# Kernel tuning notes

Hardware: AMD Instinct MI355X
Metric: run time of the kernel (lower is better)

Reference implementation:

```python
import jax, jax.numpy as jnp
import numpy as np

B, S, D, H = 2, 2048, 1024, 16
HD = D // H  # 64
SOFT_CAP = 50.0
MAX_WAVELENGTH = 10000.0


def apply_rope(x, positions, head_dim):
    # x: [B,S,H,hd], positions: [B,S]
    fraction = 2.0 * jnp.arange(head_dim // 2, dtype=jnp.float32) / head_dim
    timescale = MAX_WAVELENGTH ** fraction                      # [hd/2]
    sinusoid = positions.astype(jnp.float32)[..., None] / timescale  # [B,S,hd/2]
    sin = jnp.sin(sinusoid)[..., None, :]                       # [B,S,1,hd/2]
    cos = jnp.cos(sinusoid)[..., None, :]
    first, second = jnp.split(x, 2, axis=-1)
    out = jnp.concatenate(
        [first * cos - second * sin, second * cos + first * sin], axis=-1)
    return out.astype(x.dtype)


def setup_inputs() -> dict:
    key = jax.random.key(0)
    k1, k2, k3 = jax.random.split(key, 3)
    inputs = jax.random.normal(k1, (B, S, D), jnp.float32)
    segment_positions = jnp.tile(jnp.arange(S, dtype=jnp.int32), (B, 1))
    mask = jnp.tril(jnp.ones((S, S), dtype=bool))[None, None]   # causal [1,1,S,S]
    w_in = jax.random.normal(k2, (D, H, 3 * HD), jnp.float32) * 0.02
    w_out = jax.random.normal(k3, (H, HD, D), jnp.float32) * 0.02
    return {"inputs": inputs, "segment_positions": segment_positions,
            "mask": mask, "w_in": w_in, "w_out": w_out}


def reference(inputs, segment_positions, mask, w_in, w_out):
    # fused QKV projection: [B,S,H,3*hd]
    proj = jnp.einsum('bsd,dhe->bshe', inputs, w_in)
    q, k, v = jnp.split(proj, 3, axis=-1)
    q = apply_rope(q, segment_positions, HD)
    k = apply_rope(k, segment_positions, HD)
    q = q / jnp.sqrt(jnp.float32(HD))
    attn = jnp.einsum('bqhd,bkhd->bhqk', q, k)                  # [B,H,S,S]
    big_neg = jnp.finfo(jnp.float32).min
    attn = jnp.where(mask, attn, big_neg)
    attn = jnp.tanh(attn / SOFT_CAP) * SOFT_CAP                 # soft-cap AFTER mask
    attn = jax.nn.softmax(attn, axis=-1)
    x = jnp.einsum('bhqk,bkhd->bqhd', attn, v)
    return jnp.einsum('bqhd,hdo->bqo', x, w_out)
```

## Files before the change

kernel.cpp:

```cpp
#include <hip/hip_runtime.h>
#include <math.h>

#define BB 2
#define SS 2048
#define DD 1024
#define HH 16
#define HDIM 64
#define BS (BB*SS)
#define NQKV (HH*3*HDIM)
#define PERHEAD ((size_t)SS*HDIM)

typedef __attribute__((ext_vector_type(8))) short bf16x8;
typedef __attribute__((ext_vector_type(4))) short bf16x4;
typedef __attribute__((ext_vector_type(4))) float f32x4;

typedef const __attribute__((address_space(1))) unsigned int ga_u32;
typedef __attribute__((address_space(3))) unsigned int lds_u32;

__device__ inline short f2bf(float x) {
    union { float f; unsigned u; } v; v.f = x;
    unsigned r = v.u + 0x7FFF + ((v.u >> 16) & 1);
    return (short)(r >> 16);
}

__device__ inline void gl_lds16(const void* g, void* l) {
    __builtin_amdgcn_global_load_lds((ga_u32*)g, (lds_u32*)l, 16, 0, 0);
}

__device__ inline f32x4 mfma16(bf16x4 a, bf16x4 b, f32x4 c) {
#if __has_builtin(__builtin_amdgcn_mfma_f32_16x16x16bf16_1k)
    return __builtin_amdgcn_mfma_f32_16x16x16bf16_1k(a, b, c, 0, 0, 0);
#else
    f32x4 d;
    asm("v_mfma_f32_16x16x16_bf16 %0, %1, %2, %3"
        : "=v"(d) : "v"(a), "v"(b), "v"(c));
    return d;
#endif
}

__global__ __launch_bounds__(256)
void sincos_table(const int* __restrict__ pos, float2* __restrict__ tab)
{
    int idx = blockIdx.x * 256 + threadIdx.x;
    int i = idx & 31, s = (idx >> 5) & 2047, b = idx >> 16;
    float p  = (float)pos[b * SS + s];
    float ts = powf(10000.0f, (float)i / 32.0f);
    float sn, cs;
    sincosf(p / ts, &sn, &cs);
    tab[idx] = make_float2(cs, sn);
}

__global__ __launch_bounds__(256)
void convert_bf16(const float* __restrict__ A, unsigned short* __restrict__ Ab)
{
    int i = (blockIdx.x * 256 + threadIdx.x) * 4;
    float4 v = *(const float4*)&A[i];
    ushort4 o;
    o.x = (unsigned short)f2bf(v.x); o.y = (unsigned short)f2bf(v.y);
    o.z = (unsigned short)f2bf(v.z); o.w = (unsigned short)f2bf(v.w);
    *(ushort4*)&Ab[i] = o;
}

__global__ __launch_bounds__(256)
void transpose_bf16(const float* __restrict__ W, unsigned short* __restrict__ Wt,
                    int K, int N)
{
    __shared__ float tile[64][65];
    const int k0 = blockIdx.y * 64, n0 = blockIdx.x * 64;
    const int t = threadIdx.x;
    #pragma unroll
    for (int i = 0; i < 4; ++i) {
        int lin = t + 256 * i;
        int r = lin >> 4, c4 = (lin & 15) << 2;
        float4 v = *(const float4*)&W[(size_t)(k0 + r) * N + n0 + c4];
        tile[r][c4] = v.x; tile[r][c4 + 1] = v.y;
        tile[r][c4 + 2] = v.z; tile[r][c4 + 3] = v.w;
    }
    __syncthreads();
    #pragma unroll
    for (int i = 0; i < 4; ++i) {
        int lin = t + 256 * i;
        int n = lin >> 4, c4 = (lin & 15) << 2;
        ushort4 o;
        o.x = (unsigned short)f2bf(tile[c4 + 0][n]);
        o.y = (unsigned short)f2bf(tile[c4 + 1][n]);
        o.z = (unsigned short)f2bf(tile[c4 + 2][n]);
        o.w = (unsigned short)f2bf(tile[c4 + 3][n]);
        *(ushort4*)&Wt[(size_t)(n0 + n) * K + k0 + c4] = o;
    }
}

template<int QKV>
__global__ __launch_bounds__(256)
void gemm_mfma(const unsigned short* __restrict__ A,
               const unsigned short* __restrict__ Bt,
               float* __restrict__ C,
               unsigned short* __restrict__ Qb, unsigned short* __restrict__ Kb,
               unsigned short* __restrict__ Vb,
               const float2* __restrict__ tab,
               int M, int N, int K)
{
    __shared__ __align__(16) unsigned short As[128 * 32];
    __shared__ __align__(16) unsigned short Bs[128 * 32];
    const int t = threadIdx.x;
    const int wave = t >> 6, lane = t & 63;
    const int quad = lane >> 4, lc = lane & 15;
    const int bm = blockIdx.y * 128, bn = blockIdx.x * 128;
    const int wr = wave >> 1, wc = wave & 1;

    const int srow0 = wave * 32 + (lane >> 2);
    const int srow1 = srow0 + 16;
    const int sc = (lane & 3) ^ ((lane >> 3) & 3);
    const unsigned short* aptr0 = A  + (size_t)(bm + srow0) * K + sc * 8;
    const unsigned short* aptr1 = A  + (size_t)(bm + srow1) * K + sc * 8;
    const unsigned short* bptr0 = Bt + (size_t)(bn + srow0) * K + sc * 8;
    const unsigned short* bptr1 = Bt + (size_t)(bn + srow1) * K + sc * 8;
    unsigned short* alds0 = &As[(wave * 32)      * 32];
    unsigned short* alds1 = &As[(wave * 32 + 16) * 32];
    unsigned short* blds0 = &Bs[(wave * 32)      * 32];
    unsigned short* blds1 = &Bs[(wave * 32 + 16) * 32];

    const int cx = quad ^ ((lc >> 1) & 3);

    f32x4 acc[4][4] = {};

    for (int k0 = 0; k0 < K; k0 += 32) {
        gl_lds16(aptr0 + k0, alds0);
        gl_lds16(aptr1 + k0, alds1);
        gl_lds16(bptr0 + k0, blds0);
        gl_lds16(bptr1 + k0, blds1);
        __syncthreads();

        bf16x8 af[4], bfr[4];
        #pragma unroll
        for (int rt = 0; rt < 4; ++rt)
            af[rt] = *(const bf16x8*)&As[(wr * 64 + rt * 16 + lc) * 32 + cx * 8];
        #pragma unroll
        for (int nt = 0; nt < 4; ++nt)
            bfr[nt] = *(const bf16x8*)&Bs[(wc * 64 + nt * 16 + lc) * 32 + cx * 8];
        #pragma unroll
        for (int rt = 0; rt < 4; ++rt)
            #pragma unroll
            for (int nt = 0; nt < 4; ++nt)
                acc[rt][nt] = __builtin_amdgcn_mfma_f32_16x16x32_bf16(
                    af[rt], bfr[nt], acc[rt][nt], 0, 0, 0);
        __syncthreads();
    }

    if (QKV) {
        const int cb = blockIdx.x * 2 + wc;
        const int h = cb / 3, part = cb % 3;
        #pragma unroll
        for (int rt = 0; rt < 4; ++rt) {
            #pragma unroll
            for (int reg = 0; reg < 4; ++reg) {
                int m = bm + wr * 64 + rt * 16 + quad * 4 + reg;
                int b = m >> 11, s = m & 2047;
                if (part == 2) {
                    #pragma unroll
                    for (int nt = 0; nt < 4; ++nt) {
                        int r = nt * 16 + lc;
                        Vb[(((size_t)(b * HH + h)) * HDIM + r) * SS + s] =
                            (unsigned short)f2bf(acc[rt][nt][reg]);
                    }
                } else {
                    unsigned short* dst = part == 0 ? Qb : Kb;
                    const float scale = part == 0 ? 0.125f : 1.0f;
                    size_t rowbase = (((size_t)(b * HH + h)) * SS + s) * HDIM;
                    #pragma unroll
                    for (int nt = 0; nt < 2; ++nt) {
                        int i = nt * 16 + lc;
                        float2 cssn = tab[((size_t)(b * SS + s)) * 32 + i];
                        float first  = acc[rt][nt][reg];
                        float second = acc[rt][nt + 2][reg];
                        dst[rowbase + i] =
                            (unsigned short)f2bf((first * cssn.x - second * cssn.y) * scale);
                        dst[rowbase + i + 32] =
                            (unsigned short)f2bf((second * cssn.x + first * cssn.y) * scale);
                    }
                }
            }
        }
    } else {
        #pragma unroll
        for (int rt = 0; rt < 4; ++rt)
            #pragma unroll
            for (int reg = 0; reg < 4; ++reg) {
                int m = bm + wr * 64 + rt * 16 + quad * 4 + reg;
                #pragma unroll
                for (int nt = 0; nt < 4; ++nt) {
                    int n = bn + wc * 64 + nt * 16 + lc;
                    C[(size_t)m * N + n] = acc[rt][nt][reg];
                }
            }
    }
}

__global__ __launch_bounds__(256)
void attn_mfma_kernel(const unsigned short* __restrict__ Qb,
                      const unsigned short* __restrict__ Kb,
                      const unsigned short* __restrict__ Vb,
                      unsigned short* __restrict__ Xb)
{
    __shared__ __align__(16) unsigned short Ks[2][64 * 64];
    __shared__ __align__(16) unsigned short Vs[2][64 * 64];

    const int t    = threadIdx.x;
    const int wave = t >> 6, lane = t & 63;
    const int quad = lane >> 4, lc = lane & 15;
    const int qt   = 31 - (blockIdx.x >> 5);
    const int bh   = blockIdx.x & 31;
    const int b    = bh >> 4, h = bh & 15;

    const unsigned short* Kbase = Kb + (size_t)bh * PERHEAD;
    const unsigned short* Vbase = Vb + (size_t)bh * PERHEAD;

    const int r8 = lane >> 3, c8 = lane & 7, gcs = c8 ^ r8;

    const unsigned short* Qbase =
        Qb + ((size_t)bh * SS + (size_t)(qt * 64 + wave * 16)) * HDIM;
    bf16x8 qf[2];
    qf[0] = *(const bf16x8*)&Qbase[lc * HDIM + quad * 8];
    qf[1] = *(const bf16x8*)&Qbase[lc * HDIM + 32 + quad * 8];

    f32x4 O[4] = {{0,0,0,0},{0,0,0,0},{0,0,0,0},{0,0,0,0}};
    float l = 0.0f;

    {
        const unsigned short* ks = Kbase + (size_t)(wave * 16 + r8) * HDIM + gcs * 8;
        gl_lds16(ks,            &Ks[0][(wave * 16)     * 64]);
        gl_lds16(ks + 8 * HDIM, &Ks[0][(wave * 16 + 8) * 64]);
        const unsigned short* vs = Vbase + (size_t)(wave * 16 + r8) * SS + gcs * 8;
        gl_lds16(vs,          &Vs[0][(wave * 16)     * 64]);
        gl_lds16(vs + 8 * SS, &Vs[0][(wave * 16 + 8) * 64]);
    }

    for (int kt = 0; kt <= qt; ++kt) {
        __syncthreads();
        const int buf = kt & 1;
        if (kt < qt) {
            const int nb = buf ^ 1;
            const unsigned short* ks =
                Kbase + (size_t)((kt + 1) * 64 + wave * 16 + r8) * HDIM + gcs * 8;
            gl_lds16(ks,            &Ks[nb][(wave * 16)     * 64]);
            gl_lds16(ks + 8 * HDIM, &Ks[nb][(wave * 16 + 8) * 64]);
            const unsigned short* vs =
                Vbase + (size_t)(wave * 16 + r8) * SS + (kt + 1) * 64 + gcs * 8;
            gl_lds16(vs,          &Vs[nb][(wave * 16)     * 64]);
            gl_lds16(vs + 8 * SS, &Vs[nb][(wave * 16 + 8) * 64]);
        }

        f32x4 St[4];
        #pragma unroll
        for (int kg = 0; kg < 4; ++kg) {
            St[kg] = (f32x4){0.f, 0.f, 0.f, 0.f};
            #pragma unroll
            for (int khd = 0; khd < 2; ++khd) {
                int pc = ((khd << 2) | quad) ^ (lc & 7);
                bf16x8 kf = *(const bf16x8*)&Ks[buf][(kg * 16 + lc) * 64 + pc * 8];
                St[kg] = __builtin_amdgcn_mfma_f32_16x16x32_bf16(
                    kf, qf[khd], St[kg], 0, 0, 0);
            }
        }

        const bool diag = (kt == qt);
        bf16x4 pf[4];
        #pragma unroll
        for (int kg = 0; kg < 4; ++kg) {
            #pragma unroll
            for (int reg = 0; reg < 4; ++reg) {
                float s  = St[kg][reg];
                float s2 = s * s;
                float u  = fmaf(s2 * s, -1.92359246e-4f, s * 1.44269504f);
                float p  = __builtin_amdgcn_exp2f(u);
                if (diag && (kg * 16 + quad * 4 + reg > wave * 16 + lc)) p = 0.f;
                l += p;
                pf[kg][reg] = f2bf(p);
            }
        }

        #pragma unroll
        for (int g = 0; g < 4; ++g) {
            #pragma unroll
            for (int kg = 0; kg < 4; ++kg) {
                int pc2 = (kg * 2 + (quad >> 1)) ^ (lc & 7);
                bf16x4 vf = *(const bf16x4*)
                    &Vs[buf][(g * 16 + lc) * 64 + pc2 * 8 + (quad & 1) * 4];
                O[g] = mfma16(pf[kg], vf, O[g]);
            }
        }
    }

    l += __shfl_xor(l, 16);
    l += __shfl_xor(l, 32);
    #pragma unroll
    for (int reg = 0; reg < 4; ++reg) {
        float lq  = __shfl(l, quad * 4 + reg);
        float inv = __builtin_amdgcn_rcpf(lq);
        int q_g = qt * 64 + wave * 16 + quad * 4 + reg;
        size_t base = ((size_t)b * SS + q_g) * DD + h * HDIM;
        #pragma unroll
        for (int g = 0; g < 4; ++g)
            Xb[base + g * 16 + lc] = (unsigned short)f2bf(O[g][reg] * inv);
    }
}

extern "C" void kernel_launch(void* const* d_in, const int* in_sizes, int n_in,
                              void* d_out, int out_size, void* d_ws, size_t ws_size,
                              hipStream_t stream)
{
    const float* inputs = (const float*)d_in[0];
    const int*   pos    = (const int*)d_in[1];
    const float* w_in   = (const float*)d_in[3];
    const float* w_out  = (const float*)d_in[4];
    float* out = (float*)d_out;

    const size_t NELT = (size_t)BB * HH * SS * HDIM;
    unsigned short* Ab     = (unsigned short*)d_ws;
    unsigned short* Wt_in  = Ab + NELT;
    unsigned short* Wt_out = Wt_in + (size_t)NQKV * DD;
    unsigned short* Qb     = Wt_out + (size_t)DD * DD;
    unsigned short* Kb     = Qb + NELT;
    unsigned short* Vb     = Kb + NELT;
    unsigned short* Xb     = Vb + NELT;
    float2*         tab    = (float2*)(Xb + NELT);

    dim3 blk(256);
    sincos_table<<<dim3((BB * SS * 32) / 256), blk, 0, stream>>>(pos, tab);
    convert_bf16<<<dim3((BS * DD) / 1024), blk, 0, stream>>>(inputs, Ab);
    transpose_bf16<<<dim3(NQKV / 64, DD / 64), blk, 0, stream>>>(w_in, Wt_in, DD, NQKV);
    transpose_bf16<<<dim3(DD / 64, DD / 64), blk, 0, stream>>>(w_out, Wt_out, DD, DD);
    gemm_mfma<1><<<dim3(NQKV / 128, BS / 128), blk, 0, stream>>>(
        Ab, Wt_in, nullptr, Qb, Kb, Vb, tab, BS, NQKV, DD);
    attn_mfma_kernel<<<dim3(32 * BB * HH), blk, 0, stream>>>(Qb, Kb, Vb, Xb);
    gemm_mfma<0><<<dim3(DD / 128, BS / 128), blk, 0, stream>>>(
        Xb, Wt_out, out, nullptr, nullptr, nullptr, nullptr, BS, DD, DD);
}
```

Measured before the change: 213.5 us.

## Merge prep kernels, swap MFMA operands for V stores, narrow output GEMM tile

Merges the sin/cos table and input bf16 conversion into one launch, and the two weight transposes into one, so fewer kernel launches run. For the V part of the QKV GEMM, the MFMA operands are swapped so each lane holds consecutive head-dim values for a fixed sequence position. The transposed V stores can then be grouped more contiguously along s. The output projection GEMM now uses a 128x64 tile, doubling its grid to 512 blocks for better CU occupancy, at the cost of less B-tile reuse per block.

```diff
diff --git a/kernel.cpp b/kernel.cpp
--- a/kernel.cpp
+++ b/kernel.cpp
@@ -39,34 +39,38 @@
 }
 
 __global__ __launch_bounds__(256)
-void sincos_table(const int* __restrict__ pos, float2* __restrict__ tab)
-{
-    int idx = blockIdx.x * 256 + threadIdx.x;
-    int i = idx & 31, s = (idx >> 5) & 2047, b = idx >> 16;
-    float p  = (float)pos[b * SS + s];
-    float ts = powf(10000.0f, (float)i / 32.0f);
-    float sn, cs;
-    sincosf(p / ts, &sn, &cs);
-    tab[idx] = make_float2(cs, sn);
+void prep_kernel(const float* __restrict__ A, unsigned short* __restrict__ Ab,
+                 const int* __restrict__ pos, float2* __restrict__ tab)
+{
+    int bid = blockIdx.x, t = threadIdx.x;
+    if (bid < 4096) {
+        int i = (bid * 256 + t) * 4;
+        float4 v = *(const float4*)&A[i];
+        ushort4 o;
+        o.x = (unsigned short)f2bf(v.x); o.y = (unsigned short)f2bf(v.y);
+        o.z = (unsigned short)f2bf(v.z); o.w = (unsigned short)f2bf(v.w);
+        *(ushort4*)&Ab[i] = o;
+    } else {
+        int idx = (bid - 4096) * 256 + t;
+        int i = idx & 31, s = (idx >> 5) & 2047, b = idx >> 16;
+        float p  = (float)pos[b * SS + s];
+        float ts = powf(10000.0f, (float)i / 32.0f);
+        float sn, cs;
+        sincosf(p / ts, &sn, &cs);
+        tab[idx] = make_float2(cs, sn);
+    }
 }
 
 __global__ __launch_bounds__(256)
-void convert_bf16(const float* __restrict__ A, unsigned short* __restrict__ Ab)
-{
-    int i = (blockIdx.x * 256 + threadIdx.x) * 4;
-    float4 v = *(const float4*)&A[i];
-    ushort4 o;
-    o.x = (unsigned short)f2bf(v.x); o.y = (unsigned short)f2bf(v.y);
-    o.z = (unsigned short)f2bf(v.z); o.w = (unsigned short)f2bf(v.w);
-    *(ushort4*)&Ab[i] = o;
-}
-
-__global__ __launch_bounds__(256)
-void transpose_bf16(const float* __restrict__ W, unsigned short* __restrict__ Wt,
-                    int K, int N)
+void transpose2_bf16(const float* __restrict__ Win, unsigned short* __restrict__ Wtin,
+                     const float* __restrict__ Wout, unsigned short* __restrict__ Wtout)
 {
     __shared__ float tile[64][65];
-    const int k0 = blockIdx.y * 64, n0 = blockIdx.x * 64;
+    int id = blockIdx.x;
+    const float* W; unsigned short* Wt; int K, N, tx, ty;
+    if (id < 768) { W = Win;  Wt = Wtin;  K = DD; N = NQKV; tx = id % 48; ty = id / 48; }
+    else { id -= 768; W = Wout; Wt = Wtout; K = DD; N = DD;  tx = id % 16; ty = id / 16; }
+    const int k0 = ty * 64, n0 = tx * 64;
     const int t = threadIdx.x;
     #pragma unroll
     for (int i = 0; i < 4; ++i) {
@@ -90,7 +94,7 @@
     }
 }
 
-template<int QKV>
+template<int QKV, int NT>
 __global__ __launch_bounds__(256)
 void gemm_mfma(const unsigned short* __restrict__ A,
                const unsigned short* __restrict__ Bt,
@@ -101,71 +105,90 @@
                int M, int N, int K)
 {
     __shared__ __align__(16) unsigned short As[128 * 32];
-    __shared__ __align__(16) unsigned short Bs[128 * 32];
+    __shared__ __align__(16) unsigned short Bs[NT * 32 * 32];
     const int t = threadIdx.x;
     const int wave = t >> 6, lane = t & 63;
     const int quad = lane >> 4, lc = lane & 15;
-    const int bm = blockIdx.y * 128, bn = blockIdx.x * 128;
+    const int bm = blockIdx.y * 128, bn = blockIdx.x * (NT * 32);
     const int wr = wave >> 1, wc = wave & 1;
 
-    const int srow0 = wave * 32 + (lane >> 2);
-    const int srow1 = srow0 + 16;
+    const int cb   = blockIdx.x * 2 + wc;
+    const int h    = QKV ? (cb / 3) : 0;
+    const int part = QKV ? (cb % 3) : 0;
+    const bool vswap = QKV && (part == 2);
+
+    const int r4 = lane >> 2;
     const int sc = (lane & 3) ^ ((lane >> 3) & 3);
-    const unsigned short* aptr0 = A  + (size_t)(bm + srow0) * K + sc * 8;
-    const unsigned short* aptr1 = A  + (size_t)(bm + srow1) * K + sc * 8;
-    const unsigned short* bptr0 = Bt + (size_t)(bn + srow0) * K + sc * 8;
-    const unsigned short* bptr1 = Bt + (size_t)(bn + srow1) * K + sc * 8;
-    unsigned short* alds0 = &As[(wave * 32)      * 32];
-    unsigned short* alds1 = &As[(wave * 32 + 16) * 32];
-    unsigned short* blds0 = &Bs[(wave * 32)      * 32];
-    unsigned short* blds1 = &Bs[(wave * 32 + 16) * 32];
+    const unsigned short* aptr0 = A + (size_t)(bm + wave * 32 + r4) * K + sc * 8;
+    const unsigned short* aptr1 = aptr0 + (size_t)16 * K;
+    unsigned short* alds0 = &As[(wave * 32) * 32];
+    unsigned short* alds1 = alds0 + 16 * 32;
+    const unsigned short* bptr0 = Bt + (size_t)(bn + wave * (NT * 8) + r4) * K + sc * 8;
+    const unsigned short* bptr1 = bptr0 + (size_t)16 * K;
+    unsigned short* blds0 = &Bs[(wave * (NT * 8)) * 32];
+    unsigned short* blds1 = blds0 + 16 * 32;
 
     const int cx = quad ^ ((lc >> 1) & 3);
 
-    f32x4 acc[4][4] = {};
+    f32x4 acc[4][NT] = {};
 
     for (int k0 = 0; k0 < K; k0 += 32) {
         gl_lds16(aptr0 + k0, alds0);
         gl_lds16(aptr1 + k0, alds1);
         gl_lds16(bptr0 + k0, blds0);
-        gl_lds16(bptr1 + k0, blds1);
+        if (NT == 4) gl_lds16(bptr1 + k0, blds1);
         __syncthreads();
 
-        bf16x8 af[4], bfr[4];
+        bf16x8 af[4], bfr[NT];
         #pragma unroll
         for (int rt = 0; rt < 4; ++rt)
             af[rt] = *(const bf16x8*)&As[(wr * 64 + rt * 16 + lc) * 32 + cx * 8];
         #pragma unroll
-        for (int nt = 0; nt < 4; ++nt)
-            bfr[nt] = *(const bf16x8*)&Bs[(wc * 64 + nt * 16 + lc) * 32 + cx * 8];
-        #pragma unroll
-        for (int rt = 0; rt < 4; ++rt)
-            #pragma unroll
-            for (int nt = 0; nt < 4; ++nt)
-                acc[rt][nt] = __builtin_amdgcn_mfma_f32_16x16x32_bf16(
-                    af[rt], bfr[nt], acc[rt][nt], 0, 0, 0);
+        for (int nt = 0; nt < NT; ++nt)
+            bfr[nt] = *(const bf16x8*)&Bs[(wc * (NT * 16) + nt * 16 + lc) * 32 + cx * 8];
+        if (vswap) {
+            #pragma unroll
+            for (int rt = 0; rt < 4; ++rt)
+                #pragma unroll
+                for (int nt = 0; nt < NT; ++nt)
+                    acc[rt][nt] = __builtin_amdgcn_mfma_f32_16x16x32_bf16(
+                        bfr[nt], af[rt], acc[rt][nt], 0, 0, 0);
+        } else {
+            #pragma unroll
+            for (int rt = 0; rt < 4; ++rt)
+                #pragma unroll
+                for (int nt = 0; nt < NT; ++nt)
+                    acc[rt][nt] = __builtin_amdgcn_mfma_f32_16x16x32_bf16(
+                        af[rt], bfr[nt], acc[rt][nt], 0, 0, 0);
+        }
         __syncthreads();
     }
 
     if (QKV) {
-        const int cb = blockIdx.x * 2 + wc;
-        const int h = cb / 3, part = cb % 3;
-        #pragma unroll
-        for (int rt = 0; rt < 4; ++rt) {
-            #pragma unroll
-            for (int reg = 0; reg < 4; ++reg) {
-                int m = bm + wr * 64 + rt * 16 + quad * 4 + reg;
+        if (part == 2) {
+            #pragma unroll
+            for (int rt = 0; rt < 4; ++rt) {
+                int m = bm + wr * 64 + rt * 16 + lc;
                 int b = m >> 11, s = m & 2047;
-                if (part == 2) {
+                #pragma unroll
+                for (int nt = 0; nt < 4; ++nt) {
                     #pragma unroll
-                    for (int nt = 0; nt < 4; ++nt) {
-                        int r = nt * 16 + lc;
-                        Vb[(((size_t)(b * HH + h)) * HDIM + r) * SS + s] =
+                    for (int reg = 0; reg < 4; ++reg) {
+                        int hd = nt * 16 + quad * 4 + reg;
+                        Vb[(((size_t)(b * HH + h)) * HDIM + hd) * SS + s] =
                             (unsigned short)f2bf(acc[rt][nt][reg]);
                     }
-                } else {
-                    unsigned short* dst = part == 0 ? Qb : Kb;
-                    const float scale = part == 0 ? 0.125f : 1.0f;
+                }
+            }
+        } else {
+            unsigned short* dst = part == 0 ? Qb : Kb;
+            const float scale = part == 0 ? 0.125f : 1.0f;
+            #pragma unroll
+            for (int rt = 0; rt < 4; ++rt) {
+                #pragma unroll
+                for (int reg = 0; reg < 4; ++reg) {
+                    int m = bm + wr * 64 + rt * 16 + quad * 4 + reg;
+                    int b = m >> 11, s = m & 2047;
                     size_t rowbase = (((size_t)(b * HH + h)) * SS + s) * HDIM;
                     #pragma unroll
                     for (int nt = 0; nt < 2; ++nt) {
@@ -188,8 +211,8 @@
             for (int reg = 0; reg < 4; ++reg) {
                 int m = bm + wr * 64 + rt * 16 + quad * 4 + reg;
                 #pragma unroll
-                for (int nt = 0; nt < 4; ++nt) {
-                    int n = bn + wc * 64 + nt * 16 + lc;
+                for (int nt = 0; nt < NT; ++nt) {
+                    int n = bn + wc * (NT * 16) + nt * 16 + lc;
                     C[(size_t)m * N + n] = acc[rt][nt][reg];
                 }
             }
@@ -326,13 +349,11 @@
     float2*         tab    = (float2*)(Xb + NELT);
 
     dim3 blk(256);
-    sincos_table<<<dim3((BB * SS * 32) / 256), blk, 0, stream>>>(pos, tab);
-    convert_bf16<<<dim3((BS * DD) / 1024), blk, 0, stream>>>(inputs, Ab);
-    transpose_bf16<<<dim3(NQKV / 64, DD / 64), blk, 0, stream>>>(w_in, Wt_in, DD, NQKV);
-    transpose_bf16<<<dim3(DD / 64, DD / 64), blk, 0, stream>>>(w_out, Wt_out, DD, DD);
-    gemm_mfma<1><<<dim3(NQKV / 128, BS / 128), blk, 0, stream>>>(
+    prep_kernel<<<dim3(4096 + 512), blk, 0, stream>>>(inputs, Ab, pos, tab);
+    transpose2_bf16<<<dim3(1024), blk, 0, stream>>>(w_in, Wt_in, w_out, Wt_out);
+    gemm_mfma<1, 4><<<dim3(NQKV / 128, BS / 128), blk, 0, stream>>>(
         Ab, Wt_in, nullptr, Qb, Kb, Vb, tab, BS, NQKV, DD);
     attn_mfma_kernel<<<dim3(32 * BB * HH), blk, 0, stream>>>(Qb, Kb, Vb, Xb);
-    gemm_mfma<0><<<dim3(DD / 128, BS / 128), blk, 0, stream>>>(
+    gemm_mfma<0, 2><<<dim3(DD / 64, BS / 128), blk, 0, stream>>>(
         Xb, Wt_out, out, nullptr, nullptr, nullptr, nullptr, BS, DD, DD);
 }
```

Result: faster. 191.1 us (-10.5%).
